# Kernel tuning notes

Hardware: AMD Instinct MI355X
Metric: run time of the kernel (lower is better)

Reference implementation:

```python
import jax, jax.numpy as jnp
import numpy as np

B, T, TC = 128, 300, 20          # batch, words per sentence, chars per word
DW, DC = 16, 32                  # word / char embedding dims
UC, UM = 32, 64                  # char-LSTM units, main-LSTM units
POS, PAR = 20, 8                 # extra feature dims
VW, VC = 1834, 132               # vocab sizes
DIN = DW + UC + POS + PAR        # 76, input dim of main BiLSTM


def setup_inputs() -> dict:
    key = jax.random.key(0)
    ks = jax.random.split(key, 16)
    s = 0.05
    f32 = jnp.float32
    return dict(
        word_in=jax.random.randint(ks[0], (B, T), 0, VW, dtype=jnp.int32),
        char_in=jax.random.randint(ks[1], (B, T, TC), 0, VC, dtype=jnp.int32),
        input_pos=jax.random.normal(ks[2], (B, T, POS), f32),
        input_par=jax.random.normal(ks[3], (B, T, PAR), f32),
        emb_wor=jax.random.normal(ks[4], (VW, DW), f32) * s,
        emb_char=jax.random.normal(ks[5], (VC, DC), f32) * s,
        char_Wx=jax.random.normal(ks[6], (DC, 4 * UC), f32) * s,
        char_Wh=jax.random.normal(ks[7], (UC, 4 * UC), f32) * s,
        char_b=jnp.zeros((4 * UC,), f32),
        fwd_Wx=jax.random.normal(ks[8], (DIN, 4 * UM), f32) * s,
        fwd_Wh=jax.random.normal(ks[9], (UM, 4 * UM), f32) * s,
        fwd_b=jnp.zeros((4 * UM,), f32),
        bwd_Wx=jax.random.normal(ks[10], (DIN, 4 * UM), f32) * s,
        bwd_Wh=jax.random.normal(ks[11], (UM, 4 * UM), f32) * s,
        bwd_b=jnp.zeros((4 * UM,), f32),
        dense_W=jax.random.normal(ks[12], (2 * UM, 4), f32) * s,
        dense_b=jnp.zeros((4,), f32),
    )


def _lstm(x, mask, Wx, Wh, b):
    """Masked Keras-style LSTM (gate order i,f,g,o). x:(N,S,D) mask:(N,S) bool.
    Masked steps carry state (Keras mask_zero semantics). Returns (N,S,U)."""
    U = Wh.shape[0]
    xz = jnp.einsum('nsd,df->nsf', x, Wx) + b  # hoist input projection out of scan

    def step(carry, inp):
        h, c = carry
        z_x, m = inp
        z = z_x + h @ Wh
        i, f, g, o = jnp.split(z, 4, axis=-1)
        c_new = jax.nn.sigmoid(f) * c + jax.nn.sigmoid(i) * jnp.tanh(g)
        h_new = jax.nn.sigmoid(o) * jnp.tanh(c_new)
        m = m[:, None]
        h = jnp.where(m, h_new, h)
        c = jnp.where(m, c_new, c)
        return (h, c), h

    N = x.shape[0]
    h0 = jnp.zeros((N, U), x.dtype)
    (_, _), hs = jax.lax.scan(step, (h0, h0),
                              (jnp.swapaxes(xz, 0, 1), jnp.swapaxes(mask, 0, 1)))
    return jnp.swapaxes(hs, 0, 1)


def reference(word_in, char_in, input_pos, input_par,
              emb_wor, emb_char, char_Wx, char_Wh, char_b,
              fwd_Wx, fwd_Wh, fwd_b, bwd_Wx, bwd_Wh, bwd_b,
              dense_W, dense_b):
    # word embeddings: (B,T,DW)
    ew = emb_wor[word_in]
    # char embeddings, TimeDistributed over words: (B*T, TC, DC)
    ec = emb_char[char_in].reshape(B * T, TC, DC)
    cmask = (char_in != 0).reshape(B * T, TC)
    # char LSTM, return_sequences=False -> final (last-valid) state
    ch = _lstm(ec, cmask, char_Wx, char_Wh, char_b)[:, -1, :].reshape(B, T, UC)
    # concat word emb, char encoding, extra features -> (B,T,DIN)
    x = jnp.concatenate([ew, ch, input_pos, input_par], axis=-1)
    wmask = word_in != 0
    hf = _lstm(x, wmask, fwd_Wx, fwd_Wh, fwd_b)
    hb = _lstm(x[:, ::-1], wmask[:, ::-1], bwd_Wx, bwd_Wh, bwd_b)[:, ::-1]
    h = jnp.concatenate([hf, hb], axis=-1)  # (B,T,2*UM)
    return jax.nn.softmax(h @ dense_W + dense_b, axis=-1)  # (B,T,4)
```

## Files before the change

### kernel.cpp

```cpp
#include <hip/hip_runtime.h>
#include <hip/hip_bf16.h>

#define B_ 128
#define T_ 300
#define TC_ 20
#define DW_ 16
#define DC_ 32
#define UC_ 32
#define UM_ 64
#define POS_ 20
#define PAR_ 8
#define VW_ 1834
#define VC_ 132
#define DIN_ 76
#define XS_ 80
#define NROW (B_*T_)

typedef _Float16 half_t;
typedef half_t h2 __attribute__((ext_vector_type(2)));

__device__ __forceinline__ float fast_sig(float x){
  return __builtin_amdgcn_rcpf(1.f + __expf(-x));
}
__device__ __forceinline__ float fast_tanh(float x){
  return __builtin_amdgcn_rcpf(1.f + __expf(-2.f*x))*2.f - 1.f;
}
__device__ __forceinline__ float dot2u(unsigned int a, unsigned int b, float acc){
  union{unsigned int u; h2 h;} x, y; x.u = a; y.u = b;
#if __has_builtin(__builtin_amdgcn_fdot2)
  return __builtin_amdgcn_fdot2(x.h, y.h, acc, false);
#else
  return acc + (float)x.h.x*(float)y.h.x + (float)x.h.y*(float)y.h.y;
#endif
}
__device__ __forceinline__ float us2f(unsigned short s){
  union{unsigned short s; half_t h;} x; x.s = s; return (float)x.h;
}
__device__ __forceinline__ unsigned int packh2(float a, float b){
  union{h2 h; unsigned int u;} cv; cv.h = h2{(half_t)a,(half_t)b}; return cv.u;
}

__global__ void k_prep(const float* __restrict__ emb_char, const float* __restrict__ char_Wx,
                       const float* __restrict__ char_b,  const float* __restrict__ char_Wh,
                       const float* __restrict__ Whf, const float* __restrict__ Whb,
                       const float* __restrict__ Wxf, const float* __restrict__ Wxb,
                       float* __restrict__ xzc, half_t* __restrict__ chT,
                       half_t* __restrict__ whT_h, half_t* __restrict__ wxT_h){
  int id = blockIdx.x*256 + threadIdx.x;
  if (id < 16896){
    int v = id >> 7, j = id & 127;
    float acc = char_b[j];
    #pragma unroll
    for (int k=0;k<DC_;k++) acc += emb_char[v*DC_+k]*char_Wx[k*(4*UC_)+j];
    xzc[id] = acc;
  } else if (id < 20992){
    int t = id - 16896;
    int j = t >> 5, k = t & 31;
    chT[t] = (half_t)char_Wh[k*(4*UC_)+j];
  } else if (id < 53760){
    int t = id - 20992;
    int dirr = t >> 14, j = (t >> 6) & 255, k = t & 63;
    const float* W = dirr ? Whb : Whf;
    whT_h[t] = (half_t)W[k*(4*UM_)+j];
  } else {
    int t = id - 53760;
    int dirr = t / 24576;
    int r = t % 24576;
    int jj = r / 96, k = r % 96;
    const float* W = dirr ? Wxb : Wxf;
    wxT_h[t] = (k < DIN_) ? (half_t)W[k*(4*UM_)+jj] : (half_t)0.f;
  }
}

__global__ __launch_bounds__(512,2) void k_char(const int* __restrict__ char_in,
        const float* __restrict__ xzc, const half_t* __restrict__ chT,
        const int* __restrict__ word_in, const float* __restrict__ emb_wor,
        const float* __restrict__ pos, const float* __restrict__ par,
        float* __restrict__ x){
  __shared__ unsigned int hbuf2[8][16];
  __shared__ float2 zex[8][64];
  __shared__ int sidx[8*TC_];
  const int tid = threadIdx.x;
  const int w8 = tid >> 6;
  const int lane = tid & 63;
  const int u = lane & 31;
  const int half = lane >> 5;
  const int seq = blockIdx.x*8 + w8;

  if (tid < 384){
    int r8 = tid / 48, c48 = tid % 48;
    int row = blockIdx.x*8 + r8;
    int col = (c48 < 16) ? c48 : (c48 + 32);
    float v;
    if (col < DW_)              v = emb_wor[word_in[row]*DW_ + col];
    else if (col < DW_+UC_+POS_) v = pos[row*POS_ + (col-(DW_+UC_))];
    else                         v = par[row*PAR_ + (col-(DW_+UC_+POS_))];
    x[row*XS_ + col] = v;
  }

  if (tid < 8*TC_) sidx[tid] = char_in[blockIdx.x*(8*TC_) + tid];
  if (half==0 && u<16) hbuf2[w8][u] = 0;

  unsigned int wa[16], wb[16];
  {
    const uint4* pa = reinterpret_cast<const uint4*>(chT + (half*64+u)*32);
    const uint4* pb = reinterpret_cast<const uint4*>(chT + (half*64+32+u)*32);
    #pragma unroll
    for (int q=0;q<4;q++){
      uint4 va = pa[q], vb = pb[q];
      wa[q*4+0]=va.x; wa[q*4+1]=va.y; wa[q*4+2]=va.z; wa[q*4+3]=va.w;
      wb[q*4+0]=vb.x; wb[q*4+1]=vb.y; wb[q*4+2]=vb.z; wb[q*4+3]=vb.w;
    }
  }
  __syncthreads();

  float h = 0.f, c = 0.f;
  int idx = sidx[w8*TC_ + 0];
  float za0 = xzc[idx*(4*UC_) + half*64 + u];
  float zb0 = xzc[idx*(4*UC_) + half*64 + 32 + u];

  for (int t=0; t<TC_; t++){
    int idxn = (t+1 < TC_) ? sidx[w8*TC_ + t+1] : 0;
    float zan = xzc[idxn*(4*UC_) + half*64 + u];
    float zbn = xzc[idxn*(4*UC_) + half*64 + 32 + u];

    float za = za0, zb = zb0;
    const uint4* hb = reinterpret_cast<const uint4*>(&hbuf2[w8][0]);
    uint4 q0=hb[0], q1=hb[1], q2=hb[2], q3=hb[3];
    unsigned int hu[16] = {q0.x,q0.y,q0.z,q0.w, q1.x,q1.y,q1.z,q1.w,
                           q2.x,q2.y,q2.z,q2.w, q3.x,q3.y,q3.z,q3.w};
    #pragma unroll
    for (int k=0;k<16;k++){
      za = dot2u(wa[k], hu[k], za);
      zb = dot2u(wb[k], hu[k], zb);
    }
    zex[w8][lane] = make_float2(za, zb);
    if (half == 0){
      float2 p = zex[w8][32+u];
      float zi = za, zf = zb, zg = p.x, zo = p.y;
      float cn = fast_sig(zf)*c + fast_sig(zi)*fast_tanh(zg);
      float hn = fast_sig(zo)*fast_tanh(cn);
      bool m = (idx != 0);
      c = m ? cn : c;
      h = m ? hn : h;
      reinterpret_cast<half_t*>(&hbuf2[w8][0])[u] = (half_t)h;
    }
    idx = idxn; za0 = zan; zb0 = zbn;
  }
  if (half == 0) x[seq*XS_ + DW_ + u] = h;
}

__global__ __launch_bounds__(512,2) void k_xz(const float* __restrict__ x,
      const half_t* __restrict__ wxT_h,
      const float* __restrict__ b_f, const float* __restrict__ b_b,
      half_t* __restrict__ xz){
  __shared__ unsigned int xs[16][40];
  const int j = threadIdx.x;
  const int jj = j & 255;
  const bool bwd = (j >= 256);
  const float bj = bwd ? b_b[jj] : b_f[jj];
  const int u = jj & 63, g = jj >> 6;
  const int ocol = (bwd ? 256 : 0) + u*4 + g;

  unsigned int wq[40];
  {
    const uint4* p = reinterpret_cast<const uint4*>(wxT_h + (size_t)((bwd?256:0)+jj)*96);
    #pragma unroll
    for (int q=0;q<10;q++){
      uint4 v = p[q];
      wq[q*4+0]=v.x; wq[q*4+1]=v.y; wq[q*4+2]=v.z; wq[q*4+3]=v.w;
    }
  }

  const int rowbase = blockIdx.x*16;
  for (int i=j; i<16*40; i+=512){
    int r = i/40, q = i%40;
    unsigned int pk = 0;
    if (q < 38){
      float v0 = x[(size_t)(rowbase+r)*XS_ + 2*q];
      float v1 = x[(size_t)(rowbase+r)*XS_ + 2*q+1];
      pk = packh2(v0, v1);
    }
    xs[r][q] = pk;
  }
  __syncthreads();

  for (int r=0; r<16; r++){
    const uint4* xr = reinterpret_cast<const uint4*>(&xs[r][0]);
    float acc = bj;
    #pragma unroll
    for (int q=0;q<10;q++){
      uint4 v = xr[q];
      acc = dot2u(wq[q*4+0], v.x, acc);
      acc = dot2u(wq[q*4+1], v.y, acc);
      acc = dot2u(wq[q*4+2], v.z, acc);
      acc = dot2u(wq[q*4+3], v.w, acc);
    }
    xz[(size_t)(rowbase+r)*512 + ocol] = (half_t)acc;
  }
}

__global__ __launch_bounds__(64,1) void k_rnn(const half_t* __restrict__ xz,
      const int* __restrict__ word_in, const half_t* __restrict__ whT_h,
      float* __restrict__ hcat){
  __shared__ half_t hbuf[64];
  __shared__ int wm[T_];
  const int l = threadIdx.x;
  const int dir = blockIdx.x & 1;
  const int b = blockIdx.x >> 1;

  unsigned int wt[4][32];
  #pragma unroll
  for (int g=0; g<4; g++){
    const uint4* p = reinterpret_cast<const uint4*>(whT_h + ((size_t)dir*256 + g*64 + l)*64);
    #pragma unroll
    for (int q=0;q<8;q++){
      uint4 v = p[q];
      wt[g][q*4+0]=v.x; wt[g][q*4+1]=v.y; wt[g][q*4+2]=v.z; wt[g][q*4+3]=v.w;
    }
  }
  for (int t=l; t<T_; t+=64) wm[t] = word_in[b*T_ + (dir ? (T_-1-t) : t)];
  hbuf[l] = (half_t)0.f;
  __syncthreads();

  float h = 0.f, c_ = 0.f;
  int row0 = b*T_ + (dir ? T_-1 : 0);
  const half_t* xp = xz + (size_t)row0*512 + dir*256 + l*4;
  const ptrdiff_t dstep = dir ? -512 : 512;
  float* hout = hcat + (size_t)row0*(2*UM_) + dir*UM_ + l;
  const ptrdiff_t hstep = dir ? -(2*UM_) : (2*UM_);

  ushort4 z0 = *reinterpret_cast<const ushort4*>(xp);
  ushort4 z1 = *reinterpret_cast<const ushort4*>(xp + dstep);
  float hh[10];

  for (int outer=0; outer<30; ++outer){
    #pragma unroll
    for (int s=0; s<10; ++s){
      const int t = outer*10 + s;
      ushort4 z2 = {0,0,0,0};
      if (t+2 < T_) z2 = *reinterpret_cast<const ushort4*>(xp + 2*dstep);

      const uint4* hb = reinterpret_cast<const uint4*>(hbuf);
      float ai0=0.f, ai1=0.f, af0=0.f, af1=0.f;
      float ag0=0.f, ag1=0.f, ao0=0.f, ao1=0.f;
      #pragma unroll
      for (int q=0;q<8;q++){
        uint4 hv = hb[q];
        ai0 = dot2u(wt[0][q*4+0], hv.x, ai0); ai1 = dot2u(wt[0][q*4+1], hv.y, ai1);
        ai0 = dot2u(wt[0][q*4+2], hv.z, ai0); ai1 = dot2u(wt[0][q*4+3], hv.w, ai1);
        af0 = dot2u(wt[1][q*4+0], hv.x, af0); af1 = dot2u(wt[1][q*4+1], hv.y, af1);
        af0 = dot2u(wt[1][q*4+2], hv.z, af0); af1 = dot2u(wt[1][q*4+3], hv.w, af1);
        ag0 = dot2u(wt[2][q*4+0], hv.x, ag0); ag1 = dot2u(wt[2][q*4+1], hv.y, ag1);
        ag0 = dot2u(wt[2][q*4+2], hv.z, ag0); ag1 = dot2u(wt[2][q*4+3], hv.w, ag1);
        ao0 = dot2u(wt[3][q*4+0], hv.x, ao0); ao1 = dot2u(wt[3][q*4+1], hv.y, ao1);
        ao0 = dot2u(wt[3][q*4+2], hv.z, ao0); ao1 = dot2u(wt[3][q*4+3], hv.w, ao1);
      }
      float zi = us2f(z0.x) + (ai0+ai1);
      float zf = us2f(z0.y) + (af0+af1);
      float zg = us2f(z0.z) + (ag0+ag1);
      float zo = us2f(z0.w) + (ao0+ao1);

      int mw = wm[t];
      float cn = fast_sig(zf)*c_ + fast_sig(zi)*fast_tanh(zg);
      float hn = fast_sig(zo)*fast_tanh(cn);
      if (mw != 0){ c_ = cn; h = hn; }
      hbuf[l] = (half_t)h;
      hh[s] = h;
      z0 = z1; z1 = z2; xp += dstep;
    }
    #pragma unroll
    for (int s=0; s<10; ++s) hout[(ptrdiff_t)s * hstep] = hh[s];
    hout += (ptrdiff_t)10 * hstep;
  }
}

__global__ void k_dense(const float* __restrict__ hcat, const float* __restrict__ W,
                        const float* __restrict__ bias, float* __restrict__ out){
  int r = blockIdx.x*256 + threadIdx.x;
  const float4* h4 = reinterpret_cast<const float4*>(hcat + (size_t)r*(2*UM_));
  float a0=bias[0], a1=bias[1], a2=bias[2], a3=bias[3];
  #pragma unroll
  for (int k4=0;k4<32;k4++){
    float4 hv = h4[k4];
    float he[4] = {hv.x, hv.y, hv.z, hv.w};
    #pragma unroll
    for (int e=0;e<4;e++){
      int k = k4*4+e;
      a0 += he[e]*W[k*4+0]; a1 += he[e]*W[k*4+1];
      a2 += he[e]*W[k*4+2]; a3 += he[e]*W[k*4+3];
    }
  }
  float mx = fmaxf(fmaxf(a0,a1), fmaxf(a2,a3));
  float e0=__expf(a0-mx), e1=__expf(a1-mx), e2=__expf(a2-mx), e3=__expf(a3-mx);
  float s = __builtin_amdgcn_rcpf(e0+e1+e2+e3);
  out[r*4+0]=e0*s; out[r*4+1]=e1*s; out[r*4+2]=e2*s; out[r*4+3]=e3*s;
}

extern "C" void kernel_launch(void* const* d_in, const int* in_sizes, int n_in,
                              void* d_out, int out_size, void* d_ws, size_t ws_size,
                              hipStream_t stream) {
  const int*   word_in  = (const int*)  d_in[0];
  const int*   char_in  = (const int*)  d_in[1];
  const float* inp_pos  = (const float*)d_in[2];
  const float* inp_par  = (const float*)d_in[3];
  const float* emb_wor  = (const float*)d_in[4];
  const float* emb_char = (const float*)d_in[5];
  const float* char_Wx  = (const float*)d_in[6];
  const float* char_Wh  = (const float*)d_in[7];
  const float* char_b   = (const float*)d_in[8];
  const float* fwd_Wx   = (const float*)d_in[9];
  const float* fwd_Wh   = (const float*)d_in[10];
  const float* fwd_b    = (const float*)d_in[11];
  const float* bwd_Wx   = (const float*)d_in[12];
  const float* bwd_Wh   = (const float*)d_in[13];
  const float* bwd_b    = (const float*)d_in[14];
  const float* dense_W  = (const float*)d_in[15];
  const float* dense_b  = (const float*)d_in[16];
  float* out = (float*)d_out;

  float* xw   = (float*)d_ws;
  float* hcat = xw + (size_t)NROW*XS_;
  float* xzc  = hcat + (size_t)NROW*128;
  float* fp   = xzc + (size_t)VC_*128;
  half_t* chT   = (half_t*)fp;
  half_t* whT_h = chT + 128*32;
  half_t* wxT_h = whT_h + 2*256*64;
  half_t* xzw   = wxT_h + 2*256*96;

  k_prep <<<402, 256, 0, stream>>>(emb_char, char_Wx, char_b, char_Wh,
                                   fwd_Wh, bwd_Wh, fwd_Wx, bwd_Wx,
                                   xzc, chT, whT_h, wxT_h);
  k_char <<<NROW/8, 512, 0, stream>>>(char_in, xzc, chT,
                                      word_in, emb_wor, inp_pos, inp_par, xw);
  k_xz   <<<NROW/16, 512, 0, stream>>>(xw, wxT_h, fwd_b, bwd_b, xzw);
  k_rnn  <<<2*B_, 64, 0, stream>>>(xzw, word_in, whT_h, hcat);
  k_dense<<<NROW/256, 256, 0, stream>>>(hcat, dense_W, dense_b, out);
}
```

Baseline: 290.4 us.

## Fuse char LSTM and input projection into one kernel, widen RNN store batches

Merges the char-LSTM kernel and the xz input-projection kernel so each block builds its 8 rows of the main-LSTM input directly in shared memory (word embeddings, char final state from hbuf2, pos, par) and projects them immediately. This removes the fp32 x intermediate buffer's global write and re-read, and one kernel launch. Holding the 40-register Wx slice alongside the char-LSTM state adds register pressure and may reduce occupancy. The RNN kernel also batches hidden-state stores in groups of 15 steps instead of 10.

```diff
diff --git a/kernel.cpp b/kernel.cpp
--- a/kernel.cpp
+++ b/kernel.cpp
@@ -72,30 +72,35 @@
   }
 }
 
-__global__ __launch_bounds__(512,2) void k_char(const int* __restrict__ char_in,
+__global__ __launch_bounds__(512,2) void k_cx(const int* __restrict__ char_in,
         const float* __restrict__ xzc, const half_t* __restrict__ chT,
         const int* __restrict__ word_in, const float* __restrict__ emb_wor,
         const float* __restrict__ pos, const float* __restrict__ par,
-        float* __restrict__ x){
+        const half_t* __restrict__ wxT_h,
+        const float* __restrict__ b_f, const float* __restrict__ b_b,
+        half_t* __restrict__ xz){
   __shared__ unsigned int hbuf2[8][16];
   __shared__ float2 zex[8][64];
   __shared__ int sidx[8*TC_];
+  __shared__ unsigned int xs[8][40];
   const int tid = threadIdx.x;
   const int w8 = tid >> 6;
   const int lane = tid & 63;
   const int u = lane & 31;
   const int half = lane >> 5;
-  const int seq = blockIdx.x*8 + w8;
-
-  if (tid < 384){
-    int r8 = tid / 48, c48 = tid % 48;
-    int row = blockIdx.x*8 + r8;
-    int col = (c48 < 16) ? c48 : (c48 + 32);
-    float v;
-    if (col < DW_)              v = emb_wor[word_in[row]*DW_ + col];
-    else if (col < DW_+UC_+POS_) v = pos[row*POS_ + (col-(DW_+UC_))];
-    else                         v = par[row*PAR_ + (col-(DW_+UC_+POS_))];
-    x[row*XS_ + col] = v;
+
+  const int jj = tid & 255;
+  const bool bwd = (tid >= 256);
+  const float bj = bwd ? b_b[jj] : b_f[jj];
+  const int ocol = (bwd ? 256 : 0) + (jj & 63)*4 + (jj >> 6);
+  unsigned int wq[40];
+  {
+    const uint4* p = reinterpret_cast<const uint4*>(wxT_h + (size_t)((bwd?256:0)+jj)*96);
+    #pragma unroll
+    for (int q=0;q<10;q++){
+      uint4 v = p[q];
+      wq[q*4+0]=v.x; wq[q*4+1]=v.y; wq[q*4+2]=v.z; wq[q*4+3]=v.w;
+    }
   }
 
   if (tid < 8*TC_) sidx[tid] = char_in[blockIdx.x*(8*TC_) + tid];
@@ -147,45 +152,32 @@
     }
     idx = idxn; za0 = zan; zb0 = zbn;
   }
-  if (half == 0) x[seq*XS_ + DW_ + u] = h;
-}
-
-__global__ __launch_bounds__(512,2) void k_xz(const float* __restrict__ x,
-      const half_t* __restrict__ wxT_h,
-      const float* __restrict__ b_f, const float* __restrict__ b_b,
-      half_t* __restrict__ xz){
-  __shared__ unsigned int xs[16][40];
-  const int j = threadIdx.x;
-  const int jj = j & 255;
-  const bool bwd = (j >= 256);
-  const float bj = bwd ? b_b[jj] : b_f[jj];
-  const int u = jj & 63, g = jj >> 6;
-  const int ocol = (bwd ? 256 : 0) + u*4 + g;
-
-  unsigned int wq[40];
-  {
-    const uint4* p = reinterpret_cast<const uint4*>(wxT_h + (size_t)((bwd?256:0)+jj)*96);
-    #pragma unroll
-    for (int q=0;q<10;q++){
-      uint4 v = p[q];
-      wq[q*4+0]=v.x; wq[q*4+1]=v.y; wq[q*4+2]=v.z; wq[q*4+3]=v.w;
-    }
-  }
-
-  const int rowbase = blockIdx.x*16;
-  for (int i=j; i<16*40; i+=512){
+  __syncthreads();
+
+  for (int i=tid; i<8*40; i+=512){
     int r = i/40, q = i%40;
-    unsigned int pk = 0;
-    if (q < 38){
-      float v0 = x[(size_t)(rowbase+r)*XS_ + 2*q];
-      float v1 = x[(size_t)(rowbase+r)*XS_ + 2*q+1];
-      pk = packh2(v0, v1);
+    int row = blockIdx.x*8 + r;
+    unsigned int pk;
+    if (q < 8){
+      int wd = word_in[row];
+      pk = packh2(emb_wor[wd*DW_ + 2*q], emb_wor[wd*DW_ + 2*q+1]);
+    } else if (q < 24){
+      pk = hbuf2[r][q-8];
+    } else if (q < 34){
+      int p0 = 2*q - 48;
+      pk = packh2(pos[row*POS_ + p0], pos[row*POS_ + p0+1]);
+    } else if (q < 38){
+      int p0 = 2*q - 68;
+      pk = packh2(par[row*PAR_ + p0], par[row*PAR_ + p0+1]);
+    } else {
+      pk = 0;
     }
     xs[r][q] = pk;
   }
   __syncthreads();
 
-  for (int r=0; r<16; r++){
+  #pragma unroll
+  for (int r=0; r<8; r++){
     const uint4* xr = reinterpret_cast<const uint4*>(&xs[r][0]);
     float acc = bj;
     #pragma unroll
@@ -196,7 +188,7 @@
       acc = dot2u(wq[q*4+2], v.z, acc);
       acc = dot2u(wq[q*4+3], v.w, acc);
     }
-    xz[(size_t)(rowbase+r)*512 + ocol] = (half_t)acc;
+    xz[(size_t)(blockIdx.x*8+r)*512 + ocol] = (half_t)acc;
   }
 }
 
@@ -232,12 +224,12 @@
 
   ushort4 z0 = *reinterpret_cast<const ushort4*>(xp);
   ushort4 z1 = *reinterpret_cast<const ushort4*>(xp + dstep);
-  float hh[10];
-
-  for (int outer=0; outer<30; ++outer){
-    #pragma unroll
-    for (int s=0; s<10; ++s){
-      const int t = outer*10 + s;
+  float hh[15];
+
+  for (int outer=0; outer<20; ++outer){
+    #pragma unroll
+    for (int s=0; s<15; ++s){
+      const int t = outer*15 + s;
       ushort4 z2 = {0,0,0,0};
       if (t+2 < T_) z2 = *reinterpret_cast<const ushort4*>(xp + 2*dstep);
 
@@ -270,8 +262,8 @@
       z0 = z1; z1 = z2; xp += dstep;
     }
     #pragma unroll
-    for (int s=0; s<10; ++s) hout[(ptrdiff_t)s * hstep] = hh[s];
-    hout += (ptrdiff_t)10 * hstep;
+    for (int s=0; s<15; ++s) hout[(ptrdiff_t)s * hstep] = hh[s];
+    hout += (ptrdiff_t)15 * hstep;
   }
 }
 
@@ -319,11 +311,9 @@
   const float* dense_b  = (const float*)d_in[16];
   float* out = (float*)d_out;
 
-  float* xw   = (float*)d_ws;
-  float* hcat = xw + (size_t)NROW*XS_;
+  float* hcat = (float*)d_ws;
   float* xzc  = hcat + (size_t)NROW*128;
-  float* fp   = xzc + (size_t)VC_*128;
-  half_t* chT   = (half_t*)fp;
+  half_t* chT   = (half_t*)(xzc + (size_t)VC_*128);
   half_t* whT_h = chT + 128*32;
   half_t* wxT_h = whT_h + 2*256*64;
   half_t* xzw   = wxT_h + 2*256*96;
@@ -331,9 +321,9 @@
   k_prep <<<402, 256, 0, stream>>>(emb_char, char_Wx, char_b, char_Wh,
                                    fwd_Wh, bwd_Wh, fwd_Wx, bwd_Wx,
                                    xzc, chT, whT_h, wxT_h);
-  k_char <<<NROW/8, 512, 0, stream>>>(char_in, xzc, chT,
-                                      word_in, emb_wor, inp_pos, inp_par, xw);
-  k_xz   <<<NROW/16, 512, 0, stream>>>(xw, wxT_h, fwd_b, bwd_b, xzw);
+  k_cx   <<<NROW/8, 512, 0, stream>>>(char_in, xzc, chT,
+                                      word_in, emb_wor, inp_pos, inp_par,
+                                      wxT_h, fwd_b, bwd_b, xzw);
   k_rnn  <<<2*B_, 64, 0, stream>>>(xzw, word_in, whT_h, hcat);
   k_dense<<<NROW/256, 256, 0, stream>>>(hcat, dense_W, dense_b, out);
 }
```

Result: slower. 304.9 us (+5.0%).
